# Performance work log

Hardware: AMD Instinct MI355X
Metric: run time of the kernel (lower is better)

## Reference

```python
import jax, jax.numpy as jnp
import numpy as np

N = 50000        # nodes
E = 800000       # edges
D = 128          # input_dim
H = 128          # hidden_dim
G = 256          # graphs in batch


def setup_inputs() -> dict:
    key = jax.random.key(0)
    ks = jax.random.split(key, 9)
    x = jax.random.normal(ks[0], (N, D), dtype=jnp.float32)
    edge_index = jax.random.randint(ks[1], (2, E), 0, N, dtype=jnp.int32)
    batch = jnp.sort(jax.random.randint(ks[2], (N,), 0, G, dtype=jnp.int32))
    s0 = 1.0 / np.sqrt(D)
    s1 = 1.0 / np.sqrt(H)
    W0 = jax.random.uniform(ks[3], (D, H), jnp.float32, -s0, s0)
    b0 = jnp.zeros((H,), jnp.float32)
    alpha0 = jnp.full((H,), 0.25, jnp.float32)   # PReLU init
    W1 = jax.random.uniform(ks[4], (H, H), jnp.float32, -s1, s1)
    b1 = jnp.zeros((H,), jnp.float32)
    alpha1 = jnp.full((H,), 0.25, jnp.float32)
    return {"x": x, "edge_index": edge_index, "batch": batch,
            "W0": W0, "b0": b0, "alpha0": alpha0,
            "W1": W1, "b1": b1, "alpha1": alpha1}


def _prelu(z, alpha):
    return jnp.where(z > 0, z, alpha * z)


def reference(x, edge_index, batch, W0, b0, alpha0, W1, b1, alpha1):
    # Add self-loops (PyG GCNConv default)
    loops = jnp.arange(N, dtype=edge_index.dtype)
    src = jnp.concatenate([edge_index[0], loops])   # [E+N]
    dst = jnp.concatenate([edge_index[1], loops])   # [E+N]

    # Symmetric degree normalization: deg computed on destination (with self-loops)
    deg = jax.ops.segment_sum(jnp.ones_like(src, dtype=x.dtype), dst, num_segments=N)
    dinv = jax.lax.rsqrt(deg)                        # deg >= 1 due to self-loops
    norm = dinv[src] * dinv[dst]                     # [E+N]

    def gcn_conv(z, W, b):
        zw = z @ W                                   # [N,H] small GEMM
        msg = zw[src] * norm[:, None]                # [E+N,H] gather+scale
        return jax.ops.segment_sum(msg, dst, num_segments=N) + b

    z1 = _prelu(gcn_conv(x, W0, b0), alpha0)         # [N,H]
    z2 = _prelu(gcn_conv(z1, W1, b1), alpha1)        # [N,H]

    # global_add_pool per layer, then concat along features -> [G, 2H]
    g = jnp.concatenate([
        jax.ops.segment_sum(z1, batch, num_segments=G),
        jax.ops.segment_sum(z2, batch, num_segments=G),
    ], axis=1)
    return z2, g
```

## Files before the change

kernel.cpp:

```cpp
#include <hip/hip_runtime.h>

#define TPB 256
#define PROWS 32

typedef unsigned int uint32;
typedef unsigned short ushort16;

__device__ __forceinline__ unsigned short f2bf(float f) {
  union { float f; unsigned int i; } c; c.f = f;
  unsigned int r = c.i + 0x7fffu + ((c.i >> 16) & 1u);
  return (unsigned short)(r >> 16);
}

__device__ __forceinline__ float bflo(uint32 p) {
  union { unsigned int i; float f; } c; c.i = p << 16; return c.f;
}
__device__ __forceinline__ float bfhi(uint32 p) {
  union { unsigned int i; float f; } c; c.i = p & 0xffff0000u; return c.f;
}

__global__ void zero2_kernel(int* __restrict__ a, int na, int* __restrict__ b, int nb) {
  int i = blockIdx.x * blockDim.x + threadIdx.x;
  int stride = gridDim.x * blockDim.x;
  for (int j = i; j < na; j += stride) a[j] = 0;
  for (int j = i; j < nb; j += stride) b[j] = 0;
}

__global__ void count_rank_kernel(const int* __restrict__ dst, int E,
                                  int* __restrict__ deg, int* __restrict__ rank) {
  int i = blockIdx.x * blockDim.x + threadIdx.x;
  if (i < E) rank[i] = atomicAdd(&deg[dst[i]], 1);
}

__global__ void dinv_kernel(const int* __restrict__ deg, int n, float* __restrict__ dinv) {
  int i = blockIdx.x * blockDim.x + threadIdx.x;
  if (i < n) dinv[i] = 1.0f / sqrtf((float)(deg[i] + 1));
}

__global__ void scan_block_kernel(const int* __restrict__ in, int n,
                                  int* __restrict__ out_excl, int* __restrict__ bsum) {
  __shared__ int sh[TPB];
  int t = threadIdx.x;
  int i = blockIdx.x * TPB + t;
  int v = (i < n) ? in[i] : 0;
  sh[t] = v;
  __syncthreads();
  for (int off = 1; off < TPB; off <<= 1) {
    int x = (t >= off) ? sh[t - off] : 0;
    __syncthreads();
    sh[t] += x;
    __syncthreads();
  }
  if (i < n) out_excl[i] = sh[t] - v;
  if (t == TPB - 1 && bsum != nullptr) bsum[blockIdx.x] = sh[t];
}

__global__ void scan_fixup_kernel(int* __restrict__ rs, const int* __restrict__ boff,
                                  int n, int total) {
  int i = blockIdx.x * TPB + threadIdx.x;
  if (i < n) rs[i] += boff[blockIdx.x];
  else if (i == n) rs[n] = total;
}

__global__ void fill_kernel(const int* __restrict__ src, const int* __restrict__ dst,
                            const int* __restrict__ rank, const int* __restrict__ rs,
                            int E, int* __restrict__ col) {
  int i = blockIdx.x * blockDim.x + threadIdx.x;
  if (i < E) {
    int d = dst[i];
    col[rs[d] + rank[i]] = src[i];
  }
}

__global__ __launch_bounds__(256) void gemm128_kernel(const float* __restrict__ A,
                                                      const float* __restrict__ W,
                                                      const float* __restrict__ dinv,
                                                      ushort16* __restrict__ out, int nrows) {
  __shared__ float Wl[128 * 128];
  __shared__ float Al[32][128];
  int t = threadIdx.x;
  {
    const float4* __restrict__ W4 = (const float4*)W;
    float4* Wl4 = (float4*)Wl;
#pragma unroll
    for (int i = 0; i < 16; ++i) Wl4[t + 256 * i] = W4[t + 256 * i];
  }
  int r0 = blockIdx.x * 32;
  {
    const float4* __restrict__ A4 = (const float4*)A;
#pragma unroll
    for (int i = 0; i < 4; ++i) {
      int idx = t + 256 * i;
      int r = idx >> 5;
      int cc = idx & 31;
      float4 v = make_float4(0.f, 0.f, 0.f, 0.f);
      if (r0 + r < nrows) v = A4[(size_t)(r0 + r) * 32 + cc];
      *(float4*)&Al[r][cc * 4] = v;
    }
  }
  __syncthreads();

  int c4 = (t & 31) * 4;
  int rg = (t >> 5) * 4;
  float4 acc0 = {0, 0, 0, 0}, acc1 = {0, 0, 0, 0}, acc2 = {0, 0, 0, 0}, acc3 = {0, 0, 0, 0};
#pragma unroll 8
  for (int k = 0; k < 128; ++k) {
    float4 w = *(const float4*)&Wl[k * 128 + c4];
    float a0 = Al[rg + 0][k];
    float a1 = Al[rg + 1][k];
    float a2 = Al[rg + 2][k];
    float a3 = Al[rg + 3][k];
    acc0.x += w.x * a0; acc0.y += w.y * a0; acc0.z += w.z * a0; acc0.w += w.w * a0;
    acc1.x += w.x * a1; acc1.y += w.y * a1; acc1.z += w.z * a1; acc1.w += w.w * a1;
    acc2.x += w.x * a2; acc2.y += w.y * a2; acc2.z += w.z * a2; acc2.w += w.w * a2;
    acc3.x += w.x * a3; acc3.y += w.y * a3; acc3.z += w.z * a3; acc3.w += w.w * a3;
  }
  int r = r0 + rg;
#pragma unroll
  for (int rr = 0; rr < 4; ++rr) {
    float4 acc = (rr == 0) ? acc0 : (rr == 1) ? acc1 : (rr == 2) ? acc2 : acc3;
    if (r + rr < nrows) {
      float di = dinv[r + rr];
      ushort4 p;
      p.x = f2bf(di * acc.x); p.y = f2bf(di * acc.y);
      p.z = f2bf(di * acc.z); p.w = f2bf(di * acc.w);
      *(ushort4*)&out[(size_t)(r + rr) * 128 + c4] = p;
    }
  }
}

__global__ __launch_bounds__(256) void aggregate_kernel(
    const ushort16* __restrict__ zws, const int* __restrict__ rs,
    const int* __restrict__ col,
    const float* __restrict__ dinv, const float* __restrict__ bias,
    const float* __restrict__ alpha, float* __restrict__ out, int nrows) {
  int wid = threadIdx.x >> 6;
  int lane = threadIdx.x & 63;
  int node = blockIdx.x * 4 + wid;
  if (node >= nrows) return;
  int c = lane * 2;

  uint32 pv = *(const uint32*)&zws[(size_t)node * 128 + c];
  float accx = bflo(pv), accy = bfhi(pv);

  int e0 = rs[node], e1 = rs[node + 1];
  for (int base = e0; base < e1; base += 64) {
    int nb = e1 - base; if (nb > 64) nb = 64;
    int colv = (base + lane < e1) ? col[base + lane] : 0;
    int j = 0;
    for (; j + 8 <= nb; j += 8) {
      int s0 = __shfl(colv, j + 0);
      int s1 = __shfl(colv, j + 1);
      int s2 = __shfl(colv, j + 2);
      int s3 = __shfl(colv, j + 3);
      int s4 = __shfl(colv, j + 4);
      int s5 = __shfl(colv, j + 5);
      int s6 = __shfl(colv, j + 6);
      int s7 = __shfl(colv, j + 7);
      uint32 p0 = *(const uint32*)&zws[(size_t)s0 * 128 + c];
      uint32 p1 = *(const uint32*)&zws[(size_t)s1 * 128 + c];
      uint32 p2 = *(const uint32*)&zws[(size_t)s2 * 128 + c];
      uint32 p3 = *(const uint32*)&zws[(size_t)s3 * 128 + c];
      uint32 p4 = *(const uint32*)&zws[(size_t)s4 * 128 + c];
      uint32 p5 = *(const uint32*)&zws[(size_t)s5 * 128 + c];
      uint32 p6 = *(const uint32*)&zws[(size_t)s6 * 128 + c];
      uint32 p7 = *(const uint32*)&zws[(size_t)s7 * 128 + c];
      accx += bflo(p0) + bflo(p1) + bflo(p2) + bflo(p3)
            + bflo(p4) + bflo(p5) + bflo(p6) + bflo(p7);
      accy += bfhi(p0) + bfhi(p1) + bfhi(p2) + bfhi(p3)
            + bfhi(p4) + bfhi(p5) + bfhi(p6) + bfhi(p7);
    }
    for (; j < nb; ++j) {
      int s = __shfl(colv, j);
      uint32 p = *(const uint32*)&zws[(size_t)s * 128 + c];
      accx += bflo(p);
      accy += bfhi(p);
    }
  }

  float di = dinv[node];
  float2 b = *(const float2*)&bias[c];
  float2 al = *(const float2*)&alpha[c];
  float zx = di * accx + b.x, zy = di * accy + b.y;
  zx = zx > 0.f ? zx : al.x * zx;
  zy = zy > 0.f ? zy : al.y * zy;
  float2 r; r.x = zx; r.y = zy;
  *(float2*)&out[(size_t)node * 128 + c] = r;
}

__global__ __launch_bounds__(256) void pool_kernel(const float* __restrict__ z1,
                                                   const float* __restrict__ z2,
                                                   const int* __restrict__ batch, int n,
                                                   float* __restrict__ g) {
  int r0 = blockIdx.x * PROWS;
  int t = threadIdx.x;
  __shared__ int bsh[PROWS];
  int rmax = n - r0; if (rmax > PROWS) rmax = PROWS;
  if (t < PROWS && t < rmax) bsh[t] = batch[r0 + t];
  __syncthreads();

  int c = t & 127;
  const float* __restrict__ src = (t < 128) ? z1 : z2;
  float acc = 0.f;
  int cur = bsh[0];
  for (int i = 0; i < rmax; ++i) {
    int b = bsh[i];
    if (b != cur) {
      atomicAdd(&g[(size_t)cur * 256 + t], acc);
      acc = 0.f;
      cur = b;
    }
    acc += src[(size_t)(r0 + i) * 128 + c];
  }
  atomicAdd(&g[(size_t)cur * 256 + t], acc);
}

extern "C" void kernel_launch(void* const* d_in, const int* in_sizes, int n_in,
                              void* d_out, int out_size, void* d_ws, size_t ws_size,
                              hipStream_t stream) {
  const float* x     = (const float*)d_in[0];
  const int*   ei    = (const int*)d_in[1];
  const int*   batch = (const int*)d_in[2];
  const float* W0    = (const float*)d_in[3];
  const float* b0    = (const float*)d_in[4];
  const float* a0    = (const float*)d_in[5];
  const float* W1    = (const float*)d_in[6];
  const float* b1    = (const float*)d_in[7];
  const float* a1    = (const float*)d_in[8];
  float* out = (float*)d_out;

  const int N = in_sizes[0] / 128;
  const int E = in_sizes[1] / 2;
  const int G = (out_size - N * 128) / 256;

  const int* src  = ei;
  const int* dstp = ei + E;

  int* w = (int*)d_ws;
  size_t o = 0;
  int*      deg    = w + o; o += (size_t)N;
  int*      rs     = w + o; o += (size_t)((N + 1 + 3) & ~3);
  int*      bsum   = w + o; o += 256;
  int*      boff   = w + o; o += 256;
  int*      col    = w + o; o += (size_t)E;
  int*      rank   = w + o; o += (size_t)E;
  float*    dinv   = (float*)(w + o); o += (size_t)N;
  ushort16* zws    = (ushort16*)(w + o); o += (size_t)N * 64;
  float*    z1     = (float*)(w + o); o += (size_t)N * 128;
  (void)ws_size; (void)n_in;

  const int blkE = (E + TPB - 1) / TPB;
  const int blkN = (N + TPB - 1) / TPB;

  float* g = out + (size_t)N * 128;

  zero2_kernel<<<512, TPB, 0, stream>>>(deg, N, (int*)g, G * 256);

  count_rank_kernel<<<blkE, TPB, 0, stream>>>(dstp, E, deg, rank);
  dinv_kernel<<<blkN, TPB, 0, stream>>>(deg, N, dinv);

  scan_block_kernel<<<blkN, TPB, 0, stream>>>(deg, N, rs, bsum);
  scan_block_kernel<<<1, TPB, 0, stream>>>(bsum, blkN, boff, nullptr);
  scan_fixup_kernel<<<(N + TPB) / TPB, TPB, 0, stream>>>(rs, boff, N, E);

  fill_kernel<<<blkE, TPB, 0, stream>>>(src, dstp, rank, rs, E, col);

  gemm128_kernel<<<(N + 31) / 32, 256, 0, stream>>>(x, W0, dinv, zws, N);
  aggregate_kernel<<<(N + 3) / 4, 256, 0, stream>>>(zws, rs, col, dinv, b0, a0, z1, N);

  gemm128_kernel<<<(N + 31) / 32, 256, 0, stream>>>(z1, W1, dinv, zws, N);
  aggregate_kernel<<<(N + 3) / 4, 256, 0, stream>>>(zws, rs, col, dinv, b1, a1, out, N);

  pool_kernel<<<(N + PROWS - 1) / PROWS, 256, 0, stream>>>(z1, out, batch, N, g);
}
```

Baseline: 223.2 us.

## Replace scalar FP32 GEMM with bf16 MFMA GEMM and pre-transposed weights

Each 128x128 node-feature GEMM now runs on bf16 MFMA 16x16x32 instructions instead of scalar FP32 FMAs over shared memory. Two small kernels convert W0 and W1 to transposed bf16 up front, so B fragments are read straight from global/L2 and no 64KB weight tile is staged per block. Each block now handles 64 rows and stages results through LDS for coalesced 16-byte stores. The inputs to the GEMM are rounded to bf16, which lowers precision compared with the FP32 accumulation of the inputs before.

```diff
diff --git a/kernel.cpp b/kernel.cpp
--- a/kernel.cpp
+++ b/kernel.cpp
@@ -5,6 +5,9 @@
 
 typedef unsigned int uint32;
 typedef unsigned short ushort16;
+
+typedef __attribute__((ext_vector_type(8))) short bf16x8;
+typedef __attribute__((ext_vector_type(4))) float f32x4;
 
 __device__ __forceinline__ unsigned short f2bf(float f) {
   union { float f; unsigned int i; } c; c.f = f;
@@ -72,59 +75,78 @@
   }
 }
 
-__global__ __launch_bounds__(256) void gemm128_kernel(const float* __restrict__ A,
-                                                      const float* __restrict__ W,
-                                                      const float* __restrict__ dinv,
-                                                      ushort16* __restrict__ out, int nrows) {
-  __shared__ float Wl[128 * 128];
-  __shared__ float Al[32][128];
+__global__ void wtrans_kernel(const float* __restrict__ W, ushort16* __restrict__ wt) {
+  int i = blockIdx.x * blockDim.x + threadIdx.x;
+  int k = i >> 7;
+  int c = i & 127;
+  wt[(size_t)c * 128 + k] = f2bf(W[i]);
+}
+
+__global__ __launch_bounds__(256) void gemm_mfma_kernel(
+    const float* __restrict__ A, const ushort16* __restrict__ wt,
+    const float* __restrict__ dinv, ushort16* __restrict__ out, int nrows) {
+  __shared__ ushort16 Abf[64][128];
   int t = threadIdx.x;
-  {
-    const float4* __restrict__ W4 = (const float4*)W;
-    float4* Wl4 = (float4*)Wl;
-#pragma unroll
-    for (int i = 0; i < 16; ++i) Wl4[t + 256 * i] = W4[t + 256 * i];
-  }
-  int r0 = blockIdx.x * 32;
+  int r0 = blockIdx.x * 64;
+
   {
     const float4* __restrict__ A4 = (const float4*)A;
 #pragma unroll
-    for (int i = 0; i < 4; ++i) {
+    for (int i = 0; i < 8; ++i) {
       int idx = t + 256 * i;
       int r = idx >> 5;
       int cc = idx & 31;
       float4 v = make_float4(0.f, 0.f, 0.f, 0.f);
       if (r0 + r < nrows) v = A4[(size_t)(r0 + r) * 32 + cc];
-      *(float4*)&Al[r][cc * 4] = v;
-    }
-  }
-  __syncthreads();
-
-  int c4 = (t & 31) * 4;
-  int rg = (t >> 5) * 4;
-  float4 acc0 = {0, 0, 0, 0}, acc1 = {0, 0, 0, 0}, acc2 = {0, 0, 0, 0}, acc3 = {0, 0, 0, 0};
-#pragma unroll 8
-  for (int k = 0; k < 128; ++k) {
-    float4 w = *(const float4*)&Wl[k * 128 + c4];
-    float a0 = Al[rg + 0][k];
-    float a1 = Al[rg + 1][k];
-    float a2 = Al[rg + 2][k];
-    float a3 = Al[rg + 3][k];
-    acc0.x += w.x * a0; acc0.y += w.y * a0; acc0.z += w.z * a0; acc0.w += w.w * a0;
-    acc1.x += w.x * a1; acc1.y += w.y * a1; acc1.z += w.z * a1; acc1.w += w.w * a1;
-    acc2.x += w.x * a2; acc2.y += w.y * a2; acc2.z += w.z * a2; acc2.w += w.w * a2;
-    acc3.x += w.x * a3; acc3.y += w.y * a3; acc3.z += w.z * a3; acc3.w += w.w * a3;
-  }
-  int r = r0 + rg;
-#pragma unroll
-  for (int rr = 0; rr < 4; ++rr) {
-    float4 acc = (rr == 0) ? acc0 : (rr == 1) ? acc1 : (rr == 2) ? acc2 : acc3;
-    if (r + rr < nrows) {
-      float di = dinv[r + rr];
       ushort4 p;
-      p.x = f2bf(di * acc.x); p.y = f2bf(di * acc.y);
-      p.z = f2bf(di * acc.z); p.w = f2bf(di * acc.w);
-      *(ushort4*)&out[(size_t)(r + rr) * 128 + c4] = p;
+      p.x = f2bf(v.x); p.y = f2bf(v.y); p.z = f2bf(v.z); p.w = f2bf(v.w);
+      *(ushort4*)&Abf[r][cc * 4] = p;
+    }
+  }
+  __syncthreads();
+
+  int wave = t >> 6;
+  int lane = t & 63;
+  int lrow = lane & 15;
+  int kg = lane >> 4;
+  int rBase = wave * 16;
+
+  f32x4 acc[8];
+#pragma unroll
+  for (int ct = 0; ct < 8; ++ct) acc[ct] = (f32x4){0.f, 0.f, 0.f, 0.f};
+
+#pragma unroll
+  for (int ks = 0; ks < 4; ++ks) {
+    bf16x8 af = *(const bf16x8*)&Abf[rBase + lrow][ks * 32 + kg * 8];
+#pragma unroll
+    for (int ct = 0; ct < 8; ++ct) {
+      bf16x8 bfr = *(const bf16x8*)&wt[(size_t)(ct * 16 + lrow) * 128 + ks * 32 + kg * 8];
+      acc[ct] = __builtin_amdgcn_mfma_f32_16x16x32_bf16(af, bfr, acc[ct], 0, 0, 0);
+    }
+  }
+
+  __syncthreads();
+
+#pragma unroll
+  for (int reg = 0; reg < 4; ++reg) {
+    int rl = rBase + kg * 4 + reg;
+    int grow = r0 + rl;
+    float di = (grow < nrows) ? dinv[grow] : 0.f;
+#pragma unroll
+    for (int ct = 0; ct < 8; ++ct) {
+      Abf[rl][ct * 16 + lrow] = f2bf(di * acc[ct][reg]);
+    }
+  }
+  __syncthreads();
+
+  {
+#pragma unroll
+    for (int i = 0; i < 4; ++i) {
+      int idx = t + 256 * i;
+      int r = idx >> 4;
+      int cc = idx & 15;
+      if (r0 + r < nrows)
+        ((uint4*)&out[(size_t)(r0 + r) * 128])[cc] = ((const uint4*)&Abf[r][0])[cc];
     }
   }
 }
@@ -245,6 +267,8 @@
   int*      col    = w + o; o += (size_t)E;
   int*      rank   = w + o; o += (size_t)E;
   float*    dinv   = (float*)(w + o); o += (size_t)N;
+  ushort16* wt0    = (ushort16*)(w + o); o += 8192;
+  ushort16* wt1    = (ushort16*)(w + o); o += 8192;
   ushort16* zws    = (ushort16*)(w + o); o += (size_t)N * 64;
   float*    z1     = (float*)(w + o); o += (size_t)N * 128;
   (void)ws_size; (void)n_in;
@@ -256,6 +280,9 @@
 
   zero2_kernel<<<512, TPB, 0, stream>>>(deg, N, (int*)g, G * 256);
 
+  wtrans_kernel<<<64, TPB, 0, stream>>>(W0, wt0);
+  wtrans_kernel<<<64, TPB, 0, stream>>>(W1, wt1);
+
   count_rank_kernel<<<blkE, TPB, 0, stream>>>(dstp, E, deg, rank);
   dinv_kernel<<<blkN, TPB, 0, stream>>>(deg, N, dinv);
 
@@ -265,10 +292,10 @@
 
   fill_kernel<<<blkE, TPB, 0, stream>>>(src, dstp, rank, rs, E, col);
 
-  gemm128_kernel<<<(N + 31) / 32, 256, 0, stream>>>(x, W0, dinv, zws, N);
+  gemm_mfma_kernel<<<(N + 63) / 64, 256, 0, stream>>>(x, wt0, dinv, zws, N);
   aggregate_kernel<<<(N + 3) / 4, 256, 0, stream>>>(zws, rs, col, dinv, b0, a0, z1, N);
 
-  gemm128_kernel<<<(N + 31) / 32, 256, 0, stream>>>(z1, W1, dinv, zws, N);
+  gemm_mfma_kernel<<<(N + 63) / 64, 256, 0, stream>>>(z1, wt1, dinv, zws, N);
   aggregate_kernel<<<(N + 3) / 4, 256, 0, stream>>>(zws, rs, col, dinv, b1, a1, out, N);
 
   pool_kernel<<<(N + PROWS - 1) / PROWS, 256, 0, stream>>>(z1, out, batch, N, g);
```

Measured after the change: 206.8 us. 1.08x faster.
